# Kernel tuning notes

Hardware: AMD Instinct MI355X
Metric: run time of the kernel (lower is better)

## Reference

```python
import jax, jax.numpy as jnp
import numpy as np

B, N, DIM, H, DH = 8, 4096, 512, 8, 64
M = 266  # nb_features = int(dim_head * ln(dim_head)) = int(64*4.1589)
LN_EPS = 1e-5
K_EPS = 1e-4  # performer softmax_kernel epsilon


def _gaussian_orthogonal_matrix(m, d, rng):
    # performer_pytorch default: stacked QR blocks, rows scaled by chi(d) norms
    blocks = []
    n_full = m // d
    for _ in range(n_full):
        q, _ = np.linalg.qr(rng.standard_normal((d, d)))
        blocks.append(q.T)
    rem = m - n_full * d
    if rem > 0:
        q, _ = np.linalg.qr(rng.standard_normal((d, d)))
        blocks.append(q.T[:rem])
    proj = np.concatenate(blocks, axis=0)
    norms = np.linalg.norm(rng.standard_normal((m, d)), axis=1)
    return (proj * norms[:, None]).astype(np.float32)


def setup_inputs() -> dict:
    key = jax.random.key(0)
    ks = jax.random.split(key, 8)
    s_in = 1.0 / np.sqrt(DIM)
    s_ff = 1.0 / np.sqrt(4 * DIM)
    rng = np.random.default_rng(0)
    return {
        "x": jax.random.normal(ks[0], (B, N, DIM), jnp.float32),
        "w_q": jax.random.normal(ks[1], (DIM, DIM), jnp.float32) * s_in,
        "w_k": jax.random.normal(ks[2], (DIM, DIM), jnp.float32) * s_in,
        "w_v": jax.random.normal(ks[3], (DIM, DIM), jnp.float32) * s_in,
        "w_o": jax.random.normal(ks[4], (DIM, DIM), jnp.float32) * s_in,
        "b_o": jnp.zeros((DIM,), jnp.float32),
        "ln1_g": jnp.ones((DIM,), jnp.float32),
        "ln1_b": jnp.zeros((DIM,), jnp.float32),
        "ln2_g": jnp.ones((DIM,), jnp.float32),
        "ln2_b": jnp.zeros((DIM,), jnp.float32),
        "ff_w1": jax.random.normal(ks[5], (DIM, 4 * DIM), jnp.float32) * s_in,
        "ff_b1": jnp.zeros((4 * DIM,), jnp.float32),
        "ff_w2": jax.random.normal(ks[6], (4 * DIM, DIM), jnp.float32) * s_ff,
        "ff_b2": jnp.zeros((DIM,), jnp.float32),
        "projection": jnp.asarray(_gaussian_orthogonal_matrix(M, DH, rng)),
    }


def _layernorm(x, g, b):
    mu = jnp.mean(x, -1, keepdims=True)
    var = jnp.mean((x - mu) ** 2, -1, keepdims=True)
    return (x - mu) * jax.lax.rsqrt(var + LN_EPS) * g + b


def _softmax_kernel(data, proj, is_query):
    # FAVOR+ positive softmax-kernel features (performer_pytorch.softmax_kernel)
    dn = data.shape[-1] ** -0.25  # data_normalizer
    ratio = proj.shape[0] ** -0.5
    dd = jnp.einsum("bhnd,md->bhnm", data * dn, proj)
    diag = jnp.sum(data ** 2, -1, keepdims=True) * 0.5 * (dn ** 2)  # [B,H,N,1]
    if is_query:
        mx = jax.lax.stop_gradient(jnp.max(dd, -1, keepdims=True))
    else:
        mx = jax.lax.stop_gradient(jnp.max(dd))
    return ratio * (jnp.exp(dd - diag - mx) + K_EPS)


def reference(x, w_q, w_k, w_v, w_o, b_o, ln1_g, ln1_b, ln2_g, ln2_b,
              ff_w1, ff_b1, ff_w2, ff_b2, projection):
    # --- attention sublayer (pre-norm) ---
    h = _layernorm(x, ln1_g, ln1_b)

    def split_heads(t):
        return t.reshape(B, N, H, DH).transpose(0, 2, 1, 3)  # [B,H,N,DH]

    q = split_heads(h @ w_q)
    k = split_heads(h @ w_k)
    v = split_heads(h @ w_v)

    qp = _softmax_kernel(q, projection, True)   # [B,H,N,M]
    kp = _softmax_kernel(k, projection, False)  # [B,H,N,M]

    # non-causal linear attention: O(N) in sequence length
    d_inv = 1.0 / jnp.einsum("bhnm,bhm->bhn", qp, jnp.sum(kp, axis=2))
    ctx = jnp.einsum("bhnm,bhnd->bhmd", kp, v)          # [B,H,M,DH]
    attn = jnp.einsum("bhnm,bhmd,bhn->bhnd", qp, ctx, d_inv)
    attn = attn.transpose(0, 2, 1, 3).reshape(B, N, DIM)
    x = x + attn @ w_o + b_o

    # --- feed-forward sublayer (pre-norm) ---
    h2 = _layernorm(x, ln2_g, ln2_b)
    ff = jax.nn.gelu(h2 @ ff_w1 + ff_b1, approximate=False) @ ff_w2 + ff_b2
    return x + ff
```

## Files before the change

### kernel.cpp

```cpp
#include <hip/hip_runtime.h>
#include <cmath>

typedef unsigned short u16;
typedef unsigned int u32;
typedef short bf16x8 __attribute__((ext_vector_type(8)));
typedef float f32x4 __attribute__((ext_vector_type(4)));

#define DEVI __device__ __forceinline__

constexpr int NSEQ = 4096, DIMM = 512;
constexpr int KVLD = 1024;
constexpr int MP = 288;
constexpr int MPP = 296;
constexpr int MREAL = 266;
constexpr int DHP = 96;
constexpr float LNEPS = 1e-5f;
constexpr float KEPS = 1e-4f;
constexpr float DN = 0.3535533905932738f;
constexpr float HALF_DN2 = 0.0625f;

DEVI u16 f2bf(float f) {
  u32 u = __float_as_uint(f);
  u32 r = (u + 0x7FFFu + ((u >> 16) & 1u)) >> 16;
  return (u16)r;
}
DEVI float bf2f(u16 h) { return __uint_as_float(((u32)h) << 16); }

DEVI f32x4 mfma16(bf16x8 a, bf16x8 b, f32x4 c) {
  return __builtin_amdgcn_mfma_f32_16x16x32_bf16(a, b, c, 0, 0, 0);
}

DEVI void gload_lds16(const void* g, void* l) {
  __builtin_amdgcn_global_load_lds(
      (const __attribute__((address_space(1))) u32*)g,
      (__attribute__((address_space(3))) u32*)l, 16, 0, 0);
}

DEVI float gelu_fast(float z) {
  float a = fminf(1.5957691216057308f * (z + 0.044715f * z * z * z), 60.f);
  float e = __expf(a);
  return z * e * __builtin_amdgcn_rcpf(e + 1.f);
}

__global__ void ws_sentinel(float* out) { out[0] = 12345.0f; }

__launch_bounds__(256)
__global__ void transpose_cvt(const float* __restrict__ in, u16* __restrict__ out,
                              int K, int Nn) {
  __shared__ float tl[32][33];
  int ntn = Nn >> 5;
  int bid = blockIdx.x;
  int kt = bid / ntn, ntt = bid - kt * ntn;
  int k0 = kt << 5, nn0 = ntt << 5;
  int t = threadIdx.x;
  int r = t >> 5, c = t & 31;
#pragma unroll
  for (int i = 0; i < 4; ++i)
    tl[r + i * 8][c] = in[(size_t)(k0 + r + i * 8) * Nn + nn0 + c];
  __syncthreads();
#pragma unroll
  for (int i = 0; i < 4; ++i)
    out[(size_t)(nn0 + r + i * 8) * K + k0 + c] = f2bf(tl[c][r + i * 8]);
}

__global__ void proj_prep(const float* __restrict__ proj, u16* __restrict__ projf) {
  int idx = blockIdx.x * 256 + threadIdx.x;
  if (idx >= MP * 64) return;
  int e = idx & 7, lane = (idx >> 3) & 63, fh = idx >> 9;
  int f = fh >> 1, half = fh & 1;
  int m = f * 16 + (lane & 15);
  int d = half * 32 + (lane >> 4) * 8 + e;
  float v = (m < MREAL) ? proj[m * 64 + d] * DN : 0.f;
  projf[idx] = f2bf(v);
}

__launch_bounds__(256)
__global__ void ln_fwd(const float* __restrict__ x, const float* __restrict__ g,
                       const float* __restrict__ bt, u16* __restrict__ out) {
  int w = threadIdx.x >> 6, lane = threadIdx.x & 63;
  int row = blockIdx.x * 4 + w;
  const float* xr = x + (size_t)row * DIMM;
  int c0 = lane * 4;
  float4 v0 = *(const float4*)(xr + c0);
  float4 v1 = *(const float4*)(xr + 256 + c0);
  float s = v0.x + v0.y + v0.z + v0.w + v1.x + v1.y + v1.z + v1.w;
  float sq = v0.x * v0.x + v0.y * v0.y + v0.z * v0.z + v0.w * v0.w +
             v1.x * v1.x + v1.y * v1.y + v1.z * v1.z + v1.w * v1.w;
#pragma unroll
  for (int mk = 1; mk < 64; mk <<= 1) {
    s += __shfl_xor(s, mk, 64);
    sq += __shfl_xor(sq, mk, 64);
  }
  float mu = s * (1.f / 512.f);
  float var = sq * (1.f / 512.f) - mu * mu;
  float rstd = rsqrtf(var + LNEPS);
  float4 g0 = *(const float4*)(g + c0);
  float4 g1 = *(const float4*)(g + 256 + c0);
  float4 b0 = *(const float4*)(bt + c0);
  float4 b1 = *(const float4*)(bt + 256 + c0);
  u16* orow = out + (size_t)row * DIMM;
  uint2 p0, p1;
  {
    u16 h0 = f2bf((v0.x - mu) * rstd * g0.x + b0.x);
    u16 h1 = f2bf((v0.y - mu) * rstd * g0.y + b0.y);
    u16 h2 = f2bf((v0.z - mu) * rstd * g0.z + b0.z);
    u16 h3 = f2bf((v0.w - mu) * rstd * g0.w + b0.w);
    p0.x = ((u32)h1 << 16) | h0; p0.y = ((u32)h3 << 16) | h2;
  }
  {
    u16 h0 = f2bf((v1.x - mu) * rstd * g1.x + b1.x);
    u16 h1 = f2bf((v1.y - mu) * rstd * g1.y + b1.y);
    u16 h2 = f2bf((v1.z - mu) * rstd * g1.z + b1.z);
    u16 h3 = f2bf((v1.w - mu) * rstd * g1.w + b1.w);
    p1.x = ((u32)h1 << 16) | h0; p1.y = ((u32)h3 << 16) | h2;
  }
  *(uint2*)(orow + c0) = p0;
  *(uint2*)(orow + 256 + c0) = p1;
}

#define WAITVM(N) asm volatile("s_waitcnt vmcnt(" #N ")" ::: "memory")

template <int EPI>
__launch_bounds__(512)
__global__ void gemm256(const u16* __restrict__ A, int lda,
                        const u16* __restrict__ Bt, int ldb, int K,
                        void* __restrict__ OutP, int Nout, int ldo,
                        const float* __restrict__ bias,
                        const float* __restrict__ Res) {
  __shared__ __align__(16) u16 Al[2][256 * 64];
  __shared__ __align__(16) u16 Bl[2][256 * 64];
  int ntiles = Nout >> 8;
  int nwg = gridDim.x;
  int bid = blockIdx.x;
  int cpx = nwg >> 3;
  int wg = (bid & 7) * cpx + (bid >> 3);
  int mt = wg / ntiles, nt = wg - mt * ntiles;
  int t = threadIdx.x, lane = t & 63, w = t >> 6;
  int wm = w >> 2, wn = w & 3;
  int fr = lane & 15, fq = lane >> 4;
  int rowA0 = mt * 256, colB0 = nt * 256;
  int swz = (fr & 7) << 4;

  f32x4 acc[8][4];
#pragma unroll
  for (int i = 0; i < 8; ++i)
#pragma unroll
    for (int j = 0; j < 4; ++j) acc[i][j] = f32x4{0.f, 0.f, 0.f, 0.f};

  int srow = t >> 3;
  int so = ((t * 16) & 127) ^ ((srow & 7) << 4);

#define STAGE_A(bufi, k0)                                                       \
  do {                                                                          \
    _Pragma("unroll") for (int it = 0; it < 4; ++it) {                          \
      gload_lds16(                                                              \
          (const char*)(A + ((size_t)(rowA0 + srow + it * 64) * lda + (k0))) + so, \
          (char*)Al[bufi] + t * 16 + it * 8192);                                \
    }                                                                           \
  } while (0)
#define STAGE_B(bufi, k0)                                                       \
  do {                                                                          \
    _Pragma("unroll") for (int it = 0; it < 4; ++it) {                          \
      gload_lds16(                                                              \
          (const char*)(Bt + ((size_t)(colB0 + srow + it * 64) * ldb + (k0))) + so, \
          (char*)Bl[bufi] + t * 16 + it * 8192);                                \
    }                                                                           \
  } while (0)

  int NT = K >> 6;
  STAGE_A(0, 0);
  STAGE_B(0, 0);
  STAGE_A(1, 64);
  STAGE_B(1, 64);
  int bi = 0;
  for (int tt = 0; tt < NT; ++tt) {
    if (tt + 1 < NT) { WAITVM(8); } else { WAITVM(0); }
    __builtin_amdgcn_s_barrier();

    bf16x8 av[4][2], bv[4][2];
#pragma unroll
    for (int i = 0; i < 4; ++i)
#pragma unroll
      for (int ks = 0; ks < 2; ++ks) {
        int row = wm * 128 + i * 16 + fr;
        av[i][ks] = *(const bf16x8*)((const char*)Al[bi] + row * 128 +
                                     (((ks << 6) | (fq << 4)) ^ swz));
      }
#pragma unroll
    for (int j = 0; j < 2; ++j)
#pragma unroll
      for (int ks = 0; ks < 2; ++ks) {
        int row = wn * 64 + j * 16 + fr;
        bv[j][ks] = *(const bf16x8*)((const char*)Bl[bi] + row * 128 +
                                     (((ks << 6) | (fq << 4)) ^ swz));
      }
    __builtin_amdgcn_s_setprio(1);
#pragma unroll
    for (int i = 0; i < 4; ++i)
#pragma unroll
      for (int j = 0; j < 2; ++j)
#pragma unroll
        for (int ks = 0; ks < 2; ++ks)
          acc[i][j] = mfma16(av[i][ks], bv[j][ks], acc[i][j]);
    __builtin_amdgcn_s_setprio(0);
    __builtin_amdgcn_s_barrier();

#pragma unroll
    for (int j = 2; j < 4; ++j)
#pragma unroll
      for (int ks = 0; ks < 2; ++ks) {
        int row = wn * 64 + j * 16 + fr;
        bv[j][ks] = *(const bf16x8*)((const char*)Bl[bi] + row * 128 +
                                     (((ks << 6) | (fq << 4)) ^ swz));
      }
    __builtin_amdgcn_s_setprio(1);
#pragma unroll
    for (int i = 0; i < 4; ++i)
#pragma unroll
      for (int j = 2; j < 4; ++j)
#pragma unroll
        for (int ks = 0; ks < 2; ++ks)
          acc[i][j] = mfma16(av[i][ks], bv[j][ks], acc[i][j]);
    __builtin_amdgcn_s_setprio(0);
    asm volatile("s_waitcnt lgkmcnt(0)" ::: "memory");
    __builtin_amdgcn_sched_barrier(0);
    __builtin_amdgcn_s_barrier();
    if (tt + 2 < NT) STAGE_B(bi, (tt + 2) * 64);

#pragma unroll
    for (int i = 0; i < 4; ++i)
#pragma unroll
      for (int ks = 0; ks < 2; ++ks) {
        int row = wm * 128 + (i + 4) * 16 + fr;
        av[i][ks] = *(const bf16x8*)((const char*)Al[bi] + row * 128 +
                                     (((ks << 6) | (fq << 4)) ^ swz));
      }
    __builtin_amdgcn_s_setprio(1);
#pragma unroll
    for (int i = 0; i < 4; ++i)
#pragma unroll
      for (int j = 0; j < 2; ++j)
#pragma unroll
        for (int ks = 0; ks < 2; ++ks)
          acc[i + 4][j] = mfma16(av[i][ks], bv[j][ks], acc[i + 4][j]);
    __builtin_amdgcn_s_setprio(0);
    asm volatile("s_waitcnt lgkmcnt(0)" ::: "memory");
    __builtin_amdgcn_sched_barrier(0);
    __builtin_amdgcn_s_barrier();
    if (tt + 2 < NT) STAGE_A(bi, (tt + 2) * 64);

    __builtin_amdgcn_s_setprio(1);
#pragma unroll
    for (int i = 0; i < 4; ++i)
#pragma unroll
      for (int j = 2; j < 4; ++j)
#pragma unroll
        for (int ks = 0; ks < 2; ++ks)
          acc[i + 4][j] = mfma16(av[i][ks], bv[j][ks], acc[i + 4][j]);
    __builtin_amdgcn_s_setprio(0);
    bi ^= 1;
  }
#undef STAGE_A
#undef STAGE_B

#pragma unroll
  for (int i = 0; i < 8; ++i)
#pragma unroll
    for (int j = 0; j < 4; ++j) {
      int row = rowA0 + wm * 128 + i * 16 + fq * 4;
      int col = colB0 + wn * 64 + j * 16 + fr;
#pragma unroll
      for (int r = 0; r < 4; ++r) {
        float v = acc[i][j][r];
        size_t idx = (size_t)(row + r) * ldo + col;
        if constexpr (EPI == 0) {
          ((u16*)OutP)[idx] = f2bf(v);
        } else if constexpr (EPI == 1) {
          ((float*)OutP)[idx] = v + bias[col] + Res[(size_t)(row + r) * 512 + col];
        } else if constexpr (EPI == 2) {
          ((u16*)OutP)[idx] = f2bf(gelu_fast(v + bias[col]));
        } else {
          float bb = bias ? bias[col] : 0.f;
          ((float*)OutP)[idx] += v + bb;
        }
      }
    }
}

__launch_bounds__(256)
__global__ void kmax_kernel(const u16* __restrict__ kv, const u16* __restrict__ projf,
                            u32* __restrict__ maxslot) {
  __shared__ float wred[4];
  int bid = blockIdx.x;
  int bh = bid >> 6, nt = bid & 63;
  int b = bh >> 3, h = bh & 7;
  int n0 = nt * 64;
  int t = threadIdx.x, lane = t & 63, w = t >> 6;
  int fr = lane & 15, fq = lane >> 4;

  const u16* krow = kv + ((size_t)(b * NSEQ + n0 + w * 16 + fr)) * KVLD + h * 64;
  bf16x8 a0 = *(const bf16x8*)(krow + fq * 8);
  bf16x8 a1 = *(const bf16x8*)(krow + 32 + fq * 8);

  const bf16x8* pf = (const bf16x8*)projf;
  float m = -1e30f;
#pragma unroll
  for (int f = 0; f < 18; ++f) {
    bf16x8 b0 = pf[(f * 2 + 0) * 64 + lane];
    bf16x8 b1 = pf[(f * 2 + 1) * 64 + lane];
    f32x4 z = {0.f, 0.f, 0.f, 0.f};
    z = mfma16(a0, b0, z);
    z = mfma16(a1, b1, z);
    if (f * 16 + fr < MREAL) {
#pragma unroll
      for (int r = 0; r < 4; ++r) m = fmaxf(m, z[r]);
    }
  }
#pragma unroll
  for (int mk = 1; mk < 64; mk <<= 1) m = fmaxf(m, __shfl_xor(m, mk, 64));
  if (lane == 0) wred[w] = m;
  __syncthreads();
  if (t == 0) {
    float mm = fmaxf(fmaxf(wred[0], wred[1]), fmaxf(wred[2], wred[3]));
    u32 u = __float_as_uint(mm);
    u32 enc = (u & 0x80000000u) ? ~u : (u | 0x80000000u);
    atomicMax(maxslot, enc);
  }
}

__launch_bounds__(512)
__global__ void fused_ctx(const u16* __restrict__ kvbuf, const u16* __restrict__ projf,
                          const u32* __restrict__ maxslot, float* __restrict__ part) {
  __shared__ __align__(16) u16 kt[2][64 * 64];
  __shared__ __align__(16) u16 kpL[MP * 64];
  __shared__ __align__(16) u16 vL[DHP * 64];
  int bid = blockIdx.x;
  int bh = bid >> 2, s = bid & 3;
  int b = bh >> 3, h = bh & 7;
  int t = threadIdx.x, lane = t & 63, w = t >> 6;
  int fr = lane & 15, fq = lane >> 4;
  int rg = w & 3, fh = w >> 2;
  int wq4 = w >> 1, wn = w & 1;
  int i_base = (wq4 < 2) ? wq4 * 5 : 10 + (wq4 - 2) * 4;
  int i_cnt = (wq4 < 2) ? 5 : 4;

  if (t < 256) {
    int rr = 64 + (t >> 3), sg = t & 7;
    u16 val = (rr == 64) ? (u16)0x3F80 : (u16)0;
    uint4 v4; u16* pv = (u16*)&v4;
#pragma unroll
    for (int e = 0; e < 8; ++e) pv[e] = val;
    *(uint4*)(vL + rr * 64 + sg * 8) = v4;
  }
  u32 enc = *maxslot;
  float gmax = __uint_as_float((enc & 0x80000000u) ? (enc & 0x7FFFFFFFu) : ~enc);
  const bf16x8* pf = (const bf16x8*)projf;

  bf16x8 pfr0[9], pfr1[9];
#pragma unroll
  for (int ff = 0; ff < 9; ++ff) {
    pfr0[ff] = pf[((fh * 9 + ff) * 2 + 0) * 64 + lane];
    pfr1[ff] = pf[((fh * 9 + ff) * 2 + 1) * 64 + lane];
  }

  f32x4 acc[5][3];
#pragma unroll
  for (int i = 0; i < 5; ++i)
#pragma unroll
    for (int j = 0; j < 3; ++j) acc[i][j] = f32x4{0.f, 0.f, 0.f, 0.f};

  int str = t >> 3;
  int sch = (t & 7) ^ (str & 7);
  int vr0 = t >> 4, vsg = t & 15;
  uint2 vra, vrb;

#define KT_LOAD(ci, n0)                                                        \
  gload_lds16(kvbuf + ((size_t)(b * NSEQ + (n0) + str)) * KVLD + h * 64 + sch * 8, \
              (char*)kt[ci] + t * 16)
#define V_LOAD(n0)                                                             \
  do {                                                                         \
    vra = *(const uint2*)(kvbuf + ((size_t)(b * NSEQ + (n0) + vr0)) * KVLD + 512 + h * 64 + vsg * 4); \
    vrb = *(const uint2*)(kvbuf + ((size_t)(b * NSEQ + (n0) + vr0 + 32)) * KVLD + 512 + h * 64 + vsg * 4); \
  } while (0)

  KT_LOAD(0, s * 1024);
  V_LOAD(s * 1024);
  int cur = 0;

  for (int tile = 0; tile < 16; ++tile) {
    int n0 = s * 1024 + tile * 64;
    WAITVM(0);

    {
      u16* pv = (u16*)&vra;
#pragma unroll
      for (int e = 0; e < 4; ++e) {
        int d = vsg * 4 + e, ch = (vr0 >> 3) ^ (d & 7);
        ((u16*)((char*)vL + d * 128 + ch * 16))[vr0 & 7] = pv[e];
      }
      u16* pw = (u16*)&vrb;
      int r2 = vr0 + 32;
#pragma unroll
      for (int e = 0; e < 4; ++e) {
        int d = vsg * 4 + e, ch = (r2 >> 3) ^ (d & 7);
        ((u16*)((char*)vL + d * 128 + ch * 16))[r2 & 7] = pw[e];
      }
    }
    if (tile < 15) { KT_LOAD(cur ^ 1, n0 + 64); V_LOAD(n0 + 64); }
    asm volatile("s_waitcnt lgkmcnt(0)" ::: "memory");
    __builtin_amdgcn_s_barrier();

    int rowa = rg * 16 + fr;
    bf16x8 a0 = *(const bf16x8*)((const char*)kt[cur] + rowa * 128 +
                                 ((fq ^ (fr & 7)) << 4));
    bf16x8 a1 = *(const bf16x8*)((const char*)kt[cur] + rowa * 128 +
                                 (((4 + fq) ^ (fr & 7)) << 4));

    float ss = 0.f;
#pragma unroll
    for (int e = 0; e < 8; ++e) {
      float x0 = bf2f((u16)a0[e]), x1 = bf2f((u16)a1[e]);
      ss += x0 * x0 + x1 * x1;
    }
    ss += __shfl_xor(ss, 16, 64);
    ss += __shfl_xor(ss, 32, 64);
    float dgv[4];
#pragma unroll
    for (int r4 = 0; r4 < 4; ++r4)
      dgv[r4] = __shfl(ss, fq * 4 + r4, 64) * HALF_DN2;

#pragma unroll
    for (int ff = 0; ff < 9; ++ff) {
      int f = fh * 9 + ff;
      f32x4 z = {0.f, 0.f, 0.f, 0.f};
      z = mfma16(a0, pfr0[ff], z);
      z = mfma16(a1, pfr1[ff], z);
      int col = f * 16 + fr;
      bool ok = col < MREAL;
      float k0v = ok ? (__expf(z[0] - dgv[0] - gmax) + KEPS) : 0.f;
      float k1v = ok ? (__expf(z[1] - dgv[1] - gmax) + KEPS) : 0.f;
      float k2v = ok ? (__expf(z[2] - dgv[2] - gmax) + KEPS) : 0.f;
      float k3v = ok ? (__expf(z[3] - dgv[3] - gmax) + KEPS) : 0.f;
      u32 lo, hi;
      asm("v_cvt_pk_bf16_f32 %0, %1, %2" : "=v"(lo) : "v"(k0v), "v"(k1v));
      asm("v_cvt_pk_bf16_f32 %0, %1, %2" : "=v"(hi) : "v"(k2v), "v"(k3v));
      uint2 pk2; pk2.x = lo; pk2.y = hi;
      int ch = (rg * 2 + (fq >> 1)) ^ (fr & 7);
      *(uint2*)((char*)kpL + col * 128 + ch * 16 + (fq & 1) * 8) = pk2;
    }
    asm volatile("s_waitcnt lgkmcnt(0)" ::: "memory");
    __builtin_amdgcn_s_barrier();

#pragma unroll
    for (int kc = 0; kc < 2; ++kc) {
      int rch = ((kc * 4 + fq) ^ (fr & 7)) << 4;
      bf16x8 av[5], bv[3];
#pragma unroll
      for (int i = 0; i < 5; ++i)
        if (i < i_cnt)
          av[i] = *(const bf16x8*)((const char*)kpL + ((i_base + i) * 16 + fr) * 128 + rch);
#pragma unroll
      for (int j = 0; j < 3; ++j)
        bv[j] = *(const bf16x8*)((const char*)vL + (wn * 48 + j * 16 + fr) * 128 + rch);
#pragma unroll
      for (int i = 0; i < 5; ++i)
        if (i < i_cnt)
#pragma unroll
          for (int j = 0; j < 3; ++j) acc[i][j] = mfma16(av[i], bv[j], acc[i][j]);
    }
    asm volatile("s_waitcnt lgkmcnt(0)" ::: "memory");
    __builtin_amdgcn_s_barrier();
    cur ^= 1;
  }
#undef KT_LOAD
#undef V_LOAD

  float* dst = part + ((size_t)bh * 4 + s) * MP * DHP;
#pragma unroll
  for (int i = 0; i < 5; ++i)
    if (i < i_cnt)
#pragma unroll
      for (int j = 0; j < 3; ++j) {
        int m = (i_base + i) * 16 + fq * 4;
        int c = wn * 48 + j * 16 + fr;
#pragma unroll
        for (int r = 0; r < 4; ++r) dst[(size_t)(m + r) * DHP + c] = acc[i][j][r];
      }
}

__launch_bounds__(256)
__global__ void ctx_reduce2(const float* __restrict__ part, u16* __restrict__ ctxT) {
  int bh = blockIdx.x, t = threadIdx.x;
  const float* p = part + (size_t)bh * 4 * MP * DHP;
  u16* dst = ctxT + (size_t)bh * DHP * MP;
  for (int idx = t; idx < DHP * MP; idx += 256) {
    int d = idx / MP, m = idx - d * MP;
    size_t o = (size_t)m * DHP + d;
    float v = p[o] + p[o + MP * DHP] + p[o + 2 * MP * DHP] + p[o + 3 * MP * DHP];
    dst[idx] = f2bf(v);
  }
}

__launch_bounds__(256)
__global__ void fused_attn(const u16* __restrict__ qb, const u16* __restrict__ ctxT,
                           const u16* __restrict__ projf, u16* __restrict__ attnb) {
  __shared__ __align__(16) u16 qt[64 * 64];
  __shared__ __align__(16) u16 qpL[64 * MPP];
  __shared__ float dbuf[64];
  int bid = blockIdx.x;
  int bh = bid >> 6, nt = bid & 63;
  int b = bh >> 3, h = bh & 7;
  int n0 = nt * 64;
  int t = threadIdx.x, lane = t & 63, w = t >> 6;
  int wm = w >> 1, wn = w & 1;
  int fr = lane & 15, fq = lane >> 4;

#pragma unroll
  for (int it = 0; it < 4; ++it) {
    int idx = t + it * 256;
    int r = idx >> 4, sg = idx & 15;
    int dst = (r * 128 + sg * 8) ^ ((r & 7) << 4);
    *(uint2*)((char*)qt + dst) =
        *(const uint2*)(qb + ((size_t)(b * NSEQ + n0 + r)) * KVLD + h * 64 + sg * 4);
  }
  __syncthreads();

  int swz = (fr & 7) << 4;
  bf16x8 a0 = *(const bf16x8*)((const char*)qt +
                               (((w * 16 + fr) * 128 + fq * 16) ^ swz));
  bf16x8 a1 = *(const bf16x8*)((const char*)qt +
                               (((w * 16 + fr) * 128 + 64 + fq * 16) ^ swz));

  float ss = 0.f;
#pragma unroll
  for (int e = 0; e < 8; ++e) {
    float x0 = bf2f((u16)a0[e]), x1 = bf2f((u16)a1[e]);
    ss += x0 * x0 + x1 * x1;
  }
  ss += __shfl_xor(ss, 16, 64);
  ss += __shfl_xor(ss, 32, 64);
  float dg = ss * HALF_DN2;

  const bf16x8* pf = (const bf16x8*)projf;
  f32x4 accf[18];
#pragma unroll
  for (int f = 0; f < 18; ++f) {
    f32x4 z = {0.f, 0.f, 0.f, 0.f};
    z = mfma16(pf[(f * 2 + 0) * 64 + lane], a0, z);
    z = mfma16(pf[(f * 2 + 1) * 64 + lane], a1, z);
    accf[f] = z;
  }
  float mm = -1e30f;
#pragma unroll
  for (int f = 0; f < 18; ++f)
#pragma unroll
    for (int r = 0; r < 4; ++r) mm = fmaxf(mm, accf[f][r]);
  mm = fmaxf(mm, __shfl_xor(mm, 16, 64));
  mm = fmaxf(mm, __shfl_xor(mm, 32, 64));

  u16* qp = qpL + (w * 16 + fr) * MPP + fq * 4;
#pragma unroll
  for (int f = 0; f < 18; ++f) {
    float e0 = __expf(accf[f][0] - dg - mm) + KEPS;
    float e1 = __expf(accf[f][1] - dg - mm) + KEPS;
    float e2 = __expf(accf[f][2] - dg - mm) + KEPS;
    float e3 = __expf(accf[f][3] - dg - mm) + KEPS;
    u32 lo, hi;
    asm("v_cvt_pk_bf16_f32 %0, %1, %2" : "=v"(lo) : "v"(e0), "v"(e1));
    asm("v_cvt_pk_bf16_f32 %0, %1, %2" : "=v"(hi) : "v"(e2), "v"(e3));
    uint2 pk; pk.x = lo; pk.y = hi;
    *(uint2*)(qp + f * 16) = pk;
  }
  __syncthreads();

  const u16* cg = ctxT + (size_t)bh * DHP * MP;
  f32x4 acc2[2][3];
#pragma unroll
  for (int i = 0; i < 2; ++i)
#pragma unroll
    for (int j = 0; j < 3; ++j) acc2[i][j] = f32x4{0.f, 0.f, 0.f, 0.f};
  bf16x8 bvc[3];
#pragma unroll
  for (int j = 0; j < 3; ++j)
    bvc[j] = *(const bf16x8*)(cg + (size_t)(wn * 48 + j * 16 + fr) * MP + fq * 8);
#pragma unroll
  for (int kc = 0; kc < 9; ++kc) {
    bf16x8 bvn[3];
    if (kc < 8) {
#pragma unroll
      for (int j = 0; j < 3; ++j)
        bvn[j] = *(const bf16x8*)(cg + (size_t)(wn * 48 + j * 16 + fr) * MP +
                                  (kc + 1) * 32 + fq * 8);
    }
    bf16x8 av[2];
#pragma unroll
    for (int i = 0; i < 2; ++i)
      av[i] = *(const bf16x8*)(qpL + (wm * 32 + i * 16 + fr) * MPP + kc * 32 + fq * 8);
#pragma unroll
    for (int i = 0; i < 2; ++i)
#pragma unroll
      for (int j = 0; j < 3; ++j) acc2[i][j] = mfma16(av[i], bvc[j], acc2[i][j]);
    if (kc < 8) {
#pragma unroll
      for (int j = 0; j < 3; ++j) bvc[j] = bvn[j];
    }
  }
  if (wn == 1 && fr == 0) {
#pragma unroll
    for (int i = 0; i < 2; ++i) {
      int rl = wm * 32 + i * 16 + fq * 4;
#pragma unroll
      for (int r = 0; r < 4; ++r) dbuf[rl + r] = acc2[i][1][r];
    }
  }
  __syncthreads();

  u16* ob = qt;
#pragma unroll
  for (int i = 0; i < 2; ++i)
#pragma unroll
    for (int j = 0; j < 3; ++j) {
      int cl = wn * 48 + j * 16 + fr;
      if (cl < 64) {
        int rl = wm * 32 + i * 16 + fq * 4;
#pragma unroll
        for (int r = 0; r < 4; ++r)
          ob[(rl + r) * 64 + cl] = f2bf(acc2[i][j][r] / dbuf[rl + r]);
      }
    }
  __syncthreads();

  u16* dst = attnb + ((size_t)(b * NSEQ + n0)) * KVLD + h * 64;
  for (int idx = t; idx < 64 * 8; idx += 256) {
    int r = idx >> 3, sg = idx & 7;
    *(uint4*)(dst + (size_t)r * KVLD + sg * 8) = *(const uint4*)(ob + r * 64 + sg * 8);
  }
}

constexpr size_t OFF_WQT   = 0;
constexpr size_t OFF_WKT   = 524288;
constexpr size_t OFF_WVT   = 1048576;
constexpr size_t OFF_WOT   = 1572864;
constexpr size_t OFF_FF1T  = 2097152;
constexpr size_t OFF_FF2T  = 4194304;
constexpr size_t OFF_PROJF = 6328320;
constexpr size_t OFF_MAX   = 6365184;
constexpr size_t OFF_CTXT  = 6365440;
constexpr size_t OFF_H     = 9904384;
constexpr size_t OFF_KV    = 43458816;
constexpr size_t OFF_PART  = 110567680;
constexpr size_t WS_NEED   = 138879232;

extern "C" void kernel_launch(void* const* d_in, const int* in_sizes, int n_in,
                              void* d_out, int out_size, void* d_ws, size_t ws_size,
                              hipStream_t stream) {
  const float* x    = (const float*)d_in[0];
  const float* w_q  = (const float*)d_in[1];
  const float* w_k  = (const float*)d_in[2];
  const float* w_v  = (const float*)d_in[3];
  const float* w_o  = (const float*)d_in[4];
  const float* b_o  = (const float*)d_in[5];
  const float* ln1g = (const float*)d_in[6];
  const float* ln1b = (const float*)d_in[7];
  const float* ln2g = (const float*)d_in[8];
  const float* ln2b = (const float*)d_in[9];
  const float* ffw1 = (const float*)d_in[10];
  const float* ffb1 = (const float*)d_in[11];
  const float* ffw2 = (const float*)d_in[12];
  const float* ffb2 = (const float*)d_in[13];
  const float* proj = (const float*)d_in[14];
  (void)in_sizes; (void)n_in; (void)out_size;

  float* dout = (float*)d_out;
  if (ws_size < WS_NEED) {
    ws_sentinel<<<1, 1, 0, stream>>>(dout);
    return;
  }

  char* ws = (char*)d_ws;
  u16* wqt   = (u16*)(ws + OFF_WQT);
  u16* wkt   = (u16*)(ws + OFF_WKT);
  u16* wvt   = (u16*)(ws + OFF_WVT);
  u16* wot   = (u16*)(ws + OFF_WOT);
  u16* ff1t  = (u16*)(ws + OFF_FF1T);
  u16* ff2t  = (u16*)(ws + OFF_FF2T);
  u16* projf = (u16*)(ws + OFF_PROJF);
  u32* maxsl = (u32*)(ws + OFF_MAX);
  u16* ctxt  = (u16*)(ws + OFF_CTXT);
  u16* hbuf  = (u16*)(ws + OFF_H);
  u16* kvbuf = (u16*)(ws + OFF_KV);
  float* part = (float*)(ws + OFF_PART);

  hipMemsetAsync(maxsl, 0, 4, stream);

  transpose_cvt<<<256, 256, 0, stream>>>(w_q, wqt, 512, 512);
  transpose_cvt<<<256, 256, 0, stream>>>(w_k, wkt, 512, 512);
  transpose_cvt<<<256, 256, 0, stream>>>(w_v, wvt, 512, 512);
  transpose_cvt<<<256, 256, 0, stream>>>(w_o, wot, 512, 512);
  transpose_cvt<<<1024, 256, 0, stream>>>(ffw1, ff1t, 512, 2048);
  transpose_cvt<<<1024, 256, 0, stream>>>(ffw2, ff2t, 2048, 512);
  proj_prep<<<72, 256, 0, stream>>>(proj, projf);

  ln_fwd<<<8192, 256, 0, stream>>>(x, ln1g, ln1b, hbuf);
  gemm256<0><<<512, 512, 0, stream>>>(hbuf, 512, wkt, 512, 512, kvbuf, 1024, 1024, nullptr, nullptr);
  kmax_kernel<<<4096, 256, 0, stream>>>(kvbuf, projf, maxsl);
  fused_ctx<<<256, 512, 0, stream>>>(kvbuf, projf, maxsl, part);
  ctx_reduce2<<<64, 256, 0, stream>>>(part, ctxt);
  gemm256<0><<<256, 512, 0, stream>>>(hbuf, 512, wqt, 512, 512, kvbuf, 512, 1024, nullptr, nullptr);
  fused_attn<<<4096, 256, 0, stream>>>(kvbuf, ctxt, projf, kvbuf + 512);
  gemm256<1><<<256, 512, 0, stream>>>(kvbuf + 512, 1024, wot, 512, 512, dout, 512, 512, b_o, x);
  ln_fwd<<<8192, 256, 0, stream>>>(dout, ln2g, ln2b, hbuf);
  for (int c = 0; c < 2; ++c) {
    gemm256<2><<<512, 512, 0, stream>>>(hbuf, 512, ff1t + (size_t)c * 1024 * 512, 512, 512,
                                        kvbuf, 1024, 1024, ffb1 + c * 1024, nullptr);
    gemm256<3><<<256, 512, 0, stream>>>(kvbuf, 1024, ff2t + c * 1024, 2048, 1024,
                                        dout, 512, 512, (c == 0) ? ffb2 : nullptr, nullptr);
  }
}
```

Measured before the change: 604.0 us.

## Restructure GEMM LDS into half-tiles with finer-grained staggered prefetch schedule

```diff
diff --git a/kernel.cpp b/kernel.cpp
--- a/kernel.cpp
+++ b/kernel.cpp
@@ -119,6 +119,7 @@
 }
 
 #define WAITVM(N) asm volatile("s_waitcnt vmcnt(" #N ")" ::: "memory")
+#define LGKM0 asm volatile("s_waitcnt lgkmcnt(0)" ::: "memory")
 
 template <int EPI>
 __launch_bounds__(512)
@@ -127,8 +128,8 @@
                         void* __restrict__ OutP, int Nout, int ldo,
                         const float* __restrict__ bias,
                         const float* __restrict__ Res) {
-  __shared__ __align__(16) u16 Al[2][256 * 64];
-  __shared__ __align__(16) u16 Bl[2][256 * 64];
+  __shared__ __align__(16) u16 Al[2][2][128 * 64];
+  __shared__ __align__(16) u16 Bl[2][2][128 * 64];
   int ntiles = Nout >> 8;
   int nwg = gridDim.x;
   int bid = blockIdx.x;
@@ -140,6 +141,7 @@
   int fr = lane & 15, fq = lane >> 4;
   int rowA0 = mt * 256, colB0 = nt * 256;
   int swz = (fr & 7) << 4;
+  int hB = wn >> 1, rbB = (wn & 1) * 64;
 
   f32x4 acc[8][4];
 #pragma unroll
@@ -150,50 +152,52 @@
   int srow = t >> 3;
   int so = ((t * 16) & 127) ^ ((srow & 7) << 4);
 
-#define STAGE_A(bufi, k0)                                                       \
+#define STAGE_AH(sl, hf, k0)                                                    \
   do {                                                                          \
-    _Pragma("unroll") for (int it = 0; it < 4; ++it) {                          \
+    _Pragma("unroll") for (int it = 0; it < 2; ++it) {                          \
       gload_lds16(                                                              \
-          (const char*)(A + ((size_t)(rowA0 + srow + it * 64) * lda + (k0))) + so, \
-          (char*)Al[bufi] + t * 16 + it * 8192);                                \
+          (const char*)(A + ((size_t)(rowA0 + (hf) * 128 + srow + it * 64) * lda + (k0))) + so, \
+          (char*)Al[sl][hf] + t * 16 + it * 8192);                              \
     }                                                                           \
   } while (0)
-#define STAGE_B(bufi, k0)                                                       \
+#define STAGE_BH(sl, hf, k0)                                                    \
   do {                                                                          \
-    _Pragma("unroll") for (int it = 0; it < 4; ++it) {                          \
+    _Pragma("unroll") for (int it = 0; it < 2; ++it) {                          \
       gload_lds16(                                                              \
-          (const char*)(Bt + ((size_t)(colB0 + srow + it * 64) * ldb + (k0))) + so, \
-          (char*)Bl[bufi] + t * 16 + it * 8192);                                \
+          (const char*)(Bt + ((size_t)(colB0 + (hf) * 128 + srow + it * 64) * ldb + (k0))) + so, \
+          (char*)Bl[sl][hf] + t * 16 + it * 8192);                              \
     }                                                                           \
   } while (0)
 
   int NT = K >> 6;
-  STAGE_A(0, 0);
-  STAGE_B(0, 0);
-  STAGE_A(1, 64);
-  STAGE_B(1, 64);
-  int bi = 0;
+  STAGE_AH(0, 0, 0); STAGE_AH(0, 1, 0);
+  STAGE_BH(0, 0, 0); STAGE_BH(0, 1, 0);
+  if (NT > 1) { STAGE_AH(1, 0, 64); STAGE_AH(1, 1, 64); }
+  if (NT > 1) { WAITVM(4); } else { WAITVM(0); }
+  __builtin_amdgcn_s_barrier();
+
   for (int tt = 0; tt < NT; ++tt) {
-    if (tt + 1 < NT) { WAITVM(8); } else { WAITVM(0); }
-    __builtin_amdgcn_s_barrier();
-
+    int s = tt & 1;
+    const char* Ah = (const char*)Al[s][wm];
+    const char* Bh = (const char*)Bl[s][hB];
     bf16x8 av[4][2], bv[4][2];
+
 #pragma unroll
     for (int i = 0; i < 4; ++i)
 #pragma unroll
-      for (int ks = 0; ks < 2; ++ks) {
-        int row = wm * 128 + i * 16 + fr;
-        av[i][ks] = *(const bf16x8*)((const char*)Al[bi] + row * 128 +
+      for (int ks = 0; ks < 2; ++ks)
+        av[i][ks] = *(const bf16x8*)(Ah + (i * 16 + fr) * 128 +
                                      (((ks << 6) | (fq << 4)) ^ swz));
-      }
 #pragma unroll
     for (int j = 0; j < 2; ++j)
 #pragma unroll
-      for (int ks = 0; ks < 2; ++ks) {
-        int row = wn * 64 + j * 16 + fr;
-        bv[j][ks] = *(const bf16x8*)((const char*)Bl[bi] + row * 128 +
+      for (int ks = 0; ks < 2; ++ks)
+        bv[j][ks] = *(const bf16x8*)(Bh + (rbB + j * 16 + fr) * 128 +
                                      (((ks << 6) | (fq << 4)) ^ swz));
-      }
+    if (tt + 1 < NT) STAGE_BH(s ^ 1, 0, (tt + 1) * 64);
+    __builtin_amdgcn_s_barrier();
+    LGKM0;
+    __builtin_amdgcn_sched_barrier(0);
     __builtin_amdgcn_s_setprio(1);
 #pragma unroll
     for (int i = 0; i < 4; ++i)
@@ -208,11 +212,13 @@
 #pragma unroll
     for (int j = 2; j < 4; ++j)
 #pragma unroll
-      for (int ks = 0; ks < 2; ++ks) {
-        int row = wn * 64 + j * 16 + fr;
-        bv[j][ks] = *(const bf16x8*)((const char*)Bl[bi] + row * 128 +
+      for (int ks = 0; ks < 2; ++ks)
+        bv[j][ks] = *(const bf16x8*)(Bh + (rbB + j * 16 + fr) * 128 +
                                      (((ks << 6) | (fq << 4)) ^ swz));
-      }
+    if (tt + 1 < NT) STAGE_BH(s ^ 1, 1, (tt + 1) * 64);
+    __builtin_amdgcn_s_barrier();
+    LGKM0;
+    __builtin_amdgcn_sched_barrier(0);
     __builtin_amdgcn_s_setprio(1);
 #pragma unroll
     for (int i = 0; i < 4; ++i)
@@ -222,46 +228,44 @@
         for (int ks = 0; ks < 2; ++ks)
           acc[i][j] = mfma16(av[i][ks], bv[j][ks], acc[i][j]);
     __builtin_amdgcn_s_setprio(0);
-    asm volatile("s_waitcnt lgkmcnt(0)" ::: "memory");
+    __builtin_amdgcn_s_barrier();
+
+#pragma unroll
+    for (int i = 0; i < 4; ++i)
+#pragma unroll
+      for (int ks = 0; ks < 2; ++ks)
+        av[i][ks] = *(const bf16x8*)(Ah + (64 + i * 16 + fr) * 128 +
+                                     (((ks << 6) | (fq << 4)) ^ swz));
+    __builtin_amdgcn_s_barrier();
+    LGKM0;
     __builtin_amdgcn_sched_barrier(0);
-    __builtin_amdgcn_s_barrier();
-    if (tt + 2 < NT) STAGE_B(bi, (tt + 2) * 64);
-
+    __builtin_amdgcn_s_setprio(1);
 #pragma unroll
     for (int i = 0; i < 4; ++i)
 #pragma unroll
-      for (int ks = 0; ks < 2; ++ks) {
-        int row = wm * 128 + (i + 4) * 16 + fr;
-        av[i][ks] = *(const bf16x8*)((const char*)Al[bi] + row * 128 +
-                                     (((ks << 6) | (fq << 4)) ^ swz));
-      }
+      for (int j = 0; j < 2; ++j)
+#pragma unroll
+        for (int ks = 0; ks < 2; ++ks)
+          acc[4 + i][j] = mfma16(av[i][ks], bv[j][ks], acc[4 + i][j]);
+    __builtin_amdgcn_s_setprio(0);
+    __builtin_amdgcn_s_barrier();
+
+    if (tt + 2 < NT) { STAGE_AH(s, 0, (tt + 2) * 64); STAGE_AH(s, 1, (tt + 2) * 64); }
+    __builtin_amdgcn_s_barrier();
     __builtin_amdgcn_s_setprio(1);
 #pragma unroll
     for (int i = 0; i < 4; ++i)
 #pragma unroll
-      for (int j = 0; j < 2; ++j)
+      for (int j = 2; j < 4; ++j)
 #pragma unroll
         for (int ks = 0; ks < 2; ++ks)
-          acc[i + 4][j] = mfma16(av[i][ks], bv[j][ks], acc[i + 4][j]);
+          acc[4 + i][j] = mfma16(av[i][ks], bv[j][ks], acc[4 + i][j]);
     __builtin_amdgcn_s_setprio(0);
-    asm volatile("s_waitcnt lgkmcnt(0)" ::: "memory");
-    __builtin_amdgcn_sched_barrier(0);
-    __builtin_amdgcn_s_barrier();
-    if (tt + 2 < NT) STAGE_A(bi, (tt + 2) * 64);
-
-    __builtin_amdgcn_s_setprio(1);
-#pragma unroll
-    for (int i = 0; i < 4; ++i)
-#pragma unroll
-      for (int j = 2; j < 4; ++j)
-#pragma unroll
-        for (int ks = 0; ks < 2; ++ks)
-          acc[i + 4][j] = mfma16(av[i][ks], bv[j][ks], acc[i + 4][j]);
-    __builtin_amdgcn_s_setprio(0);
-    bi ^= 1;
-  }
-#undef STAGE_A
-#undef STAGE_B
+    if (tt + 2 < NT) { WAITVM(4); } else if (tt + 1 < NT) { WAITVM(0); }
+    __builtin_amdgcn_s_barrier();
+  }
+#undef STAGE_AH
+#undef STAGE_BH
 
 #pragma unroll
   for (int i = 0; i < 8; ++i)
```

After: 621.5 us. +2.9%, slower.
